# Kernel optimization log

Hardware: AMD Instinct MI355X
Metric: run time of the kernel (lower is better)

The kernel has to match this reference:

```python
import jax, jax.numpy as jnp
import numpy as np

HQ, HK, HD, DM = 16, 8, 128, 2048
GQA = HQ // HK
SCALE = HD ** -0.5


def _rotate_half(x):
    half = x.shape[-1] // 2
    return jnp.concatenate([-x[..., half:], x[..., :half]], axis=-1)


def _rope_tables(T, d, base=10000.0):
    inv_freq = 1.0 / (base ** (np.arange(0, d // 2, dtype=np.float32) * 2.0 / d))
    ang = np.arange(T, dtype=np.float32)[:, None] * inv_freq[None, :]  # [T, d/2]
    ang = np.concatenate([ang, ang], axis=-1)                          # [T, d]
    cos = jnp.asarray(np.cos(ang))[None, None]                         # [1,1,T,d]
    sin = jnp.asarray(np.sin(ang))[None, None]
    return cos, sin


def setup_inputs() -> dict:
    key = jax.random.key(0)
    ks = jax.random.split(key, 8)
    B, T, L = 1, 2048, 4
    x = jax.random.normal(ks[0], (B, T, DM), dtype=jnp.float32)
    depth_k = jax.random.normal(ks[1], (L, B, HK, T, HD), dtype=jnp.float32)
    depth_v = jax.random.normal(ks[2], (L, B, HK, T, HD), dtype=jnp.float32)
    cos, sin = _rope_tables(T, HD)
    Wq = jax.random.normal(ks[3], (DM, HQ * HD), dtype=jnp.float32) * 0.02
    Wk = jax.random.normal(ks[4], (DM, HK * HD), dtype=jnp.float32) * 0.02
    Wv = jax.random.normal(ks[5], (DM, HK * HD), dtype=jnp.float32) * 0.02
    Wo = jax.random.normal(ks[6], (HQ * HD, DM), dtype=jnp.float32) * 0.02
    return {"x": x, "depth_k": depth_k, "depth_v": depth_v, "cos": cos, "sin": sin,
            "Wq": Wq, "Wk": Wk, "Wv": Wv, "Wo": Wo}


def reference(x, depth_k, depth_v, cos, sin, Wq, Wk, Wv, Wo):
    B, T, D = x.shape
    # Projections -> [B, H, T, d]
    Q = (x @ Wq).reshape(B, T, HQ, HD).transpose(0, 2, 1, 3)
    K = (x @ Wk).reshape(B, T, HK, HD).transpose(0, 2, 1, 3)
    V = (x @ Wv).reshape(B, T, HK, HD).transpose(0, 2, 1, 3)
    # RoPE
    Q = Q * cos + _rotate_half(Q) * sin
    K = K * cos + _rotate_half(K) * sin
    # GQA expand (repeat_interleave along head axis)
    K_e = jnp.repeat(K, GQA, axis=1)
    V_e = jnp.repeat(V, GQA, axis=1)
    # Sequence logits with causal mask: [B, Hq, T, T]
    seq_logits = jnp.einsum('bhid,bhjd->bhij', Q, K_e) * SCALE
    causal = jnp.triu(jnp.ones((T, T), dtype=bool), k=1)
    seq_logits = jnp.where(causal[None, None], -jnp.inf, seq_logits)
    # Depth KVs: [L,B,Hk,T,d] -> [B,Hk,T,L,d] -> expand heads
    Kd = jnp.repeat(jnp.transpose(depth_k, (1, 2, 3, 0, 4)), GQA, axis=1)
    Vd = jnp.repeat(jnp.transpose(depth_v, (1, 2, 3, 0, 4)), GQA, axis=1)
    depth_logits = jnp.einsum('bhid,bhild->bhil', Q, Kd) * SCALE  # [B,Hq,T,L]
    # Joint softmax over sequence + depth positions
    combined = jnp.concatenate([seq_logits, depth_logits], axis=-1)
    weights = jax.nn.softmax(combined, axis=-1)
    seq_contrib = jnp.einsum('bhij,bhjd->bhid', weights[..., :T], V_e)
    depth_contrib = jnp.einsum('bhil,bhild->bhid', weights[..., T:], Vd)
    out = (seq_contrib + depth_contrib).transpose(0, 2, 1, 3).reshape(B, T, HQ * HD)
    return out @ Wo
```

## Files before the change

kernel.cpp:

```cpp
#include <hip/hip_runtime.h>
#include <hip/hip_bf16.h>
#include <math.h>

#define T_SEQ 2048
#define DMODEL 2048
#define NHQ 16
#define NHK 8
#define HDIM 128
#define NL 4
#define ATT_SCALE 0.08838834764831845f

typedef __attribute__((ext_vector_type(8))) short bf16x8;
typedef __attribute__((ext_vector_type(4))) float f32x4;

__device__ __forceinline__ float bf2f(short u) {
    union { float f; unsigned int i; } x;
    x.i = ((unsigned int)(unsigned short)u) << 16;
    return x.f;
}
__device__ __forceinline__ unsigned short f2bf(float f) {
    __hip_bfloat16 h = __float2bfloat16(f);
    return *reinterpret_cast<unsigned short*>(&h);
}
__device__ __forceinline__ void gload16(const void* g, void* l) {
    __builtin_amdgcn_global_load_lds(
        (const __attribute__((address_space(1))) void*)g,
        (__attribute__((address_space(3))) void*)l, 16, 0, 0);
}

__global__ __launch_bounds__(256) void prep(
    const float* __restrict__ x, const float* __restrict__ Wq,
    const float* __restrict__ Wk, const float* __restrict__ Wv,
    const float* __restrict__ Wo,
    unsigned short* __restrict__ xb, unsigned short* __restrict__ WTp,
    unsigned short* __restrict__ WoT)
{
    __shared__ float ls[64][65];
    const int bid = blockIdx.x, tid = threadIdx.x;
    if (bid < 2048) {
        int i = bid * 256 + tid;
        float4 a = ((const float4*)x)[2 * i];
        float4 b = ((const float4*)x)[2 * i + 1];
        bf16x8 v;
        v[0] = (short)f2bf(a.x); v[1] = (short)f2bf(a.y);
        v[2] = (short)f2bf(a.z); v[3] = (short)f2bf(a.w);
        v[4] = (short)f2bf(b.x); v[5] = (short)f2bf(b.y);
        v[6] = (short)f2bf(b.z); v[7] = (short)f2bf(b.w);
        ((bf16x8*)xb)[i] = v;
        return;
    }
    int v = bid - 2048;
    const float* src; unsigned short* dst; int Nsrc, dstOff, id;
    if (v < 1024)      { src = Wq; dst = WTp; Nsrc = 2048; dstOff = 0;    id = v; }
    else if (v < 1536) { src = Wk; dst = WTp; Nsrc = 1024; dstOff = 2048; id = v - 1024; }
    else if (v < 2048) { src = Wv; dst = WTp; Nsrc = 1024; dstOff = 3072; id = v - 1536; }
    else               { src = Wo; dst = WoT; Nsrc = 2048; dstOff = 0;    id = v - 2048; }
    const int k0 = (id & 31) * 64, n0 = (id >> 5) * 64;
    #pragma unroll
    for (int it = 0; it < 4; ++it) {
        int fi = tid + it * 256;
        int r = fi >> 4;
        int c = (fi & 15) * 4;
        float4 w = *(const float4*)&src[(size_t)(k0 + r) * Nsrc + n0 + c];
        ls[r][c] = w.x; ls[r][c + 1] = w.y; ls[r][c + 2] = w.z; ls[r][c + 3] = w.w;
    }
    __syncthreads();
    int n = tid & 63, kc = tid >> 6;
    bf16x8 v0, v1;
    #pragma unroll
    for (int j = 0; j < 8; ++j) v0[j] = (short)f2bf(ls[kc * 16 + j][n]);
    #pragma unroll
    for (int j = 0; j < 8; ++j) v1[j] = (short)f2bf(ls[kc * 16 + 8 + j][n]);
    size_t drow = (size_t)(dstOff + n0 + n) * 2048 + k0 + kc * 16;
    *(bf16x8*)&dst[drow] = v0;
    *(bf16x8*)&dst[drow + 8] = v1;
}

__global__ __launch_bounds__(256, 4) void gemm_bt(
    const unsigned short* __restrict__ A, const unsigned short* __restrict__ Bt,
    float* __restrict__ Cf, unsigned short* __restrict__ Cq,
    unsigned short* __restrict__ Ck, unsigned short* __restrict__ Cv,
    int mode, int K)
{
    __shared__ char As[16384];
    __shared__ char Bs[8192];
    const int tid = threadIdx.x;
    const int wv = tid >> 6, lane = tid & 63;
    const int l15 = lane & 15, lg = lane >> 4;
    const int wm = wv >> 1, wn = wv & 1;
    const int bm = blockIdx.y * 128, bn = blockIdx.x * 64;

    f32x4 acc[4][2];
    #pragma unroll
    for (int i = 0; i < 4; ++i)
        #pragma unroll
        for (int j = 0; j < 2; ++j)
            acc[i][j] = (f32x4){0.f, 0.f, 0.f, 0.f};

    for (int k0 = 0; k0 < K; k0 += 64) {
        #pragma unroll
        for (int it = 0; it < 4; ++it) {
            int o = it * 4096 + tid * 16;
            int row = o >> 7;
            int sch = ((o >> 4) & 7) ^ (row & 7);
            gload16((const char*)A + ((((size_t)(bm + row) * K) + k0 + sch * 8) << 1),
                    As + it * 4096 + wv * 1024);
        }
        #pragma unroll
        for (int it = 0; it < 2; ++it) {
            int o = it * 4096 + tid * 16;
            int row = o >> 7;
            int sch = ((o >> 4) & 7) ^ (row & 7);
            gload16((const char*)Bt + ((((size_t)(bn + row) * K) + k0 + sch * 8) << 1),
                    Bs + it * 4096 + wv * 1024);
        }
        __syncthreads();
        #pragma unroll
        for (int kk = 0; kk < 2; ++kk) {
            bf16x8 av[4], bv[2];
            #pragma unroll
            for (int f = 0; f < 4; ++f) {
                int ra = wm * 64 + f * 16 + l15;
                av[f] = *(const bf16x8*)(As + ra * 128 + ((((kk << 2) | lg) ^ (ra & 7)) << 4));
            }
            #pragma unroll
            for (int f = 0; f < 2; ++f) {
                int rb = wn * 32 + f * 16 + l15;
                bv[f] = *(const bf16x8*)(Bs + rb * 128 + ((((kk << 2) | lg) ^ (rb & 7)) << 4));
            }
            #pragma unroll
            for (int mf = 0; mf < 4; ++mf)
                #pragma unroll
                for (int nf = 0; nf < 2; ++nf)
                    acc[mf][nf] = __builtin_amdgcn_mfma_f32_16x16x32_bf16(
                        av[mf], bv[nf], acc[mf][nf], 0, 0, 0);
        }
        __syncthreads();
    }

    #pragma unroll
    for (int mf = 0; mf < 4; ++mf) {
        int m0 = bm + wm * 64 + mf * 16 + lg * 4;
        #pragma unroll
        for (int nf = 0; nf < 2; ++nf) {
            int n0 = bn + wn * 32 + nf * 16 + l15;
            if (mode == 0) {
                #pragma unroll
                for (int r = 0; r < 4; ++r)
                    Cf[(size_t)(m0 + r) * 2048 + n0] = acc[mf][nf][r];
            } else if (n0 < 2048) {
                #pragma unroll
                for (int r = 0; r < 4; ++r)
                    Cq[(size_t)(m0 + r) * 2048 + n0] = f2bf(acc[mf][nf][r]);
            } else if (n0 < 3072) {
                #pragma unroll
                for (int r = 0; r < 4; ++r)
                    Ck[(size_t)(m0 + r) * 1024 + (n0 - 2048)] = f2bf(acc[mf][nf][r]);
            } else {
                ushort4 u;
                u.x = f2bf(acc[mf][nf][0]); u.y = f2bf(acc[mf][nf][1]);
                u.z = f2bf(acc[mf][nf][2]); u.w = f2bf(acc[mf][nf][3]);
                *(ushort4*)&Cv[(size_t)(n0 - 3072) * 2048 + m0] = u;
            }
        }
    }
}

__global__ __launch_bounds__(256) void rope2(
    unsigned short* __restrict__ Qb, unsigned short* __restrict__ Kb,
    const float* __restrict__ cosT, const float* __restrict__ sinT)
{
    int idx = blockIdx.x * 256 + threadIdx.x;
    unsigned short* P; int H;
    if (idx < T_SEQ * NHQ * 64) { P = Qb; H = NHQ; }
    else { idx -= T_SEQ * NHQ * 64; P = Kb; H = NHK; }
    int d = idx & 63;
    int h = (idx >> 6) % H;
    int t = idx / (64 * H);
    float c = cosT[t * HDIM + d];
    float s = sinT[t * HDIM + d];
    unsigned short* row = P + (size_t)t * (H * HDIM) + h * HDIM;
    float x0 = bf2f((short)row[d]), x1 = bf2f((short)row[d + 64]);
    row[d]      = f2bf(x0 * c - x1 * s);
    row[d + 64] = f2bf(x1 * c + x0 * s);
}

__global__ __launch_bounds__(256) void depth_part(
    const unsigned short* __restrict__ Qb,
    const float* __restrict__ Dk, const float* __restrict__ Dv,
    unsigned short* __restrict__ Opart, float2* __restrict__ mlpart)
{
    const int bid = blockIdx.x;
    const int hk = bid & 7;
    const int tc = bid >> 3;
    const int tid = threadIdx.x;
    const int row = tid >> 3;
    const int dp = tid & 7;
    const int t = tc * 32 + row;
    const int qt = t >> 6, rowin = t & 63;
    const size_t DSTRIDE = (size_t)NHK * T_SEQ * HDIM;
    const size_t base = ((size_t)hk * T_SEQ + t) * HDIM + dp * 16;

    float q[2][16];
    #pragma unroll
    for (int e = 0; e < 2; ++e) {
        const unsigned short* qp = Qb + (size_t)t * DMODEL + (hk * 2 + e) * HDIM + dp * 16;
        bf16x8 v0 = *(const bf16x8*)qp;
        bf16x8 v1 = *(const bf16x8*)(qp + 8);
        #pragma unroll
        for (int j = 0; j < 8; ++j) { q[e][j] = bf2f(v0[j]); q[e][8 + j] = bf2f(v1[j]); }
    }
    float dl[2][NL];
    #pragma unroll
    for (int l = 0; l < NL; ++l) {
        const float* kp = Dk + l * DSTRIDE + base;
        float a0 = 0.f, a1 = 0.f;
        #pragma unroll
        for (int c = 0; c < 4; ++c) {
            float4 k4 = *(const float4*)(kp + c * 4);
            a0 = fmaf(q[0][c*4+0], k4.x, a0); a0 = fmaf(q[0][c*4+1], k4.y, a0);
            a0 = fmaf(q[0][c*4+2], k4.z, a0); a0 = fmaf(q[0][c*4+3], k4.w, a0);
            a1 = fmaf(q[1][c*4+0], k4.x, a1); a1 = fmaf(q[1][c*4+1], k4.y, a1);
            a1 = fmaf(q[1][c*4+2], k4.z, a1); a1 = fmaf(q[1][c*4+3], k4.w, a1);
        }
        a0 += __shfl_xor(a0, 1); a0 += __shfl_xor(a0, 2); a0 += __shfl_xor(a0, 4);
        a1 += __shfl_xor(a1, 1); a1 += __shfl_xor(a1, 2); a1 += __shfl_xor(a1, 4);
        dl[0][l] = a0 * ATT_SCALE;
        dl[1][l] = a1 * ATT_SCALE;
    }
    float m[2], ls[2], pd[2][NL];
    #pragma unroll
    for (int e = 0; e < 2; ++e) {
        m[e] = fmaxf(fmaxf(dl[e][0], dl[e][1]), fmaxf(dl[e][2], dl[e][3]));
        ls[e] = 0.f;
        #pragma unroll
        for (int l = 0; l < NL; ++l) { pd[e][l] = __expf(dl[e][l] - m[e]); ls[e] += pd[e][l]; }
    }
    float o[2][16];
    #pragma unroll
    for (int e = 0; e < 2; ++e)
        #pragma unroll
        for (int j = 0; j < 16; ++j) o[e][j] = 0.f;
    #pragma unroll
    for (int l = 0; l < NL; ++l) {
        const float* vp = Dv + l * DSTRIDE + base;
        #pragma unroll
        for (int c = 0; c < 4; ++c) {
            float4 v4 = *(const float4*)(vp + c * 4);
            #pragma unroll
            for (int e = 0; e < 2; ++e) {
                o[e][c*4+0] = fmaf(pd[e][l], v4.x, o[e][c*4+0]);
                o[e][c*4+1] = fmaf(pd[e][l], v4.y, o[e][c*4+1]);
                o[e][c*4+2] = fmaf(pd[e][l], v4.z, o[e][c*4+2]);
                o[e][c*4+3] = fmaf(pd[e][l], v4.w, o[e][c*4+3]);
            }
        }
    }
    #pragma unroll
    for (int e = 0; e < 2; ++e) {
        int pidx = ((hk * 2 + e) * 32 + qt) * 5 + 4;
        unsigned short* dst = Opart + (size_t)pidx * 8192 + rowin * 128 + dp * 16;
        bf16x8 w0, w1;
        #pragma unroll
        for (int j = 0; j < 8; ++j) { w0[j] = (short)f2bf(o[e][j]); w1[j] = (short)f2bf(o[e][8 + j]); }
        *(bf16x8*)dst = w0;
        *(bf16x8*)(dst + 8) = w1;
        if (dp == 0) mlpart[pidx * 64 + rowin] = make_float2(m[e], ls[e]);
    }
}

__global__ __launch_bounds__(256, 5) void attn_seg(
    const unsigned short* __restrict__ Qb, const unsigned short* __restrict__ Kb,
    const unsigned short* __restrict__ Vt,
    unsigned short* __restrict__ Opart, float2* __restrict__ mlpart)
{
    __shared__ char Ks[2][8192];
    __shared__ char Vs[2][8192];

    const int bid = blockIdx.x;
    const int hk = bid & 7;
    const int idx = bid >> 3;
    const int hq = hk * 2 + (idx & 1);
    const int si = 79 - (idx >> 1);
    int qt, seg;
    if (si < 8)       { qt = si;            seg = 0; }
    else if (si < 24) { int v = si - 8;  qt = 8  + (v >> 1); seg = v & 1; }
    else if (si < 48) { int v = si - 24; int q3 = v / 3; qt = 16 + q3; seg = v - q3 * 3; }
    else              { int v = si - 48; qt = 24 + (v >> 2); seg = v & 3; }
    const int q0 = qt * 64;
    const int keys = q0 + 64;
    const int jbeg = seg * 512;
    const int jend = min(jbeg + 512, keys);

    const int tid = threadIdx.x;
    const int wv = tid >> 6, lane = tid & 63;
    const int l15 = lane & 15, lg = lane >> 4;

    const int tq = q0 + wv * 16 + l15;
    const int qmax = q0 + wv * 16 + 15;
    const int qmin = q0 + wv * 16;

    bf16x8 qf[4];
    {
        const unsigned short* qrow = Qb + (size_t)tq * DMODEL + hq * HDIM;
        #pragma unroll
        for (int c = 0; c < 4; ++c)
            qf[c] = *(const bf16x8*)(qrow + c * 32 + lg * 8);
    }

    f32x4 oacc[8];
    #pragma unroll
    for (int dt = 0; dt < 8; ++dt) oacc[dt] = (f32x4){0.f, 0.f, 0.f, 0.f};
    float m = -1e30f, l = 0.f;

    #define STAGE(J0, BUF)                                                        \
        {                                                                         \
            _Pragma("unroll")                                                     \
            for (int it = 0; it < 2; ++it) {                                      \
                int o = it * 4096 + tid * 16;                                     \
                int rk = o >> 8, ck = (o >> 4) & 15;                              \
                gload16((const char*)Kb +                                         \
                        (((size_t)((J0) + rk) * 1024 + hk * 128 +                 \
                          ((ck ^ (rk & 7)) << 3)) << 1),                          \
                        Ks[BUF] + it * 4096 + wv * 1024);                         \
                int rv = o >> 6, cv = (o >> 4) & 3;                               \
                gload16((const char*)Vt +                                         \
                        (((size_t)(hk * 128 + rv) * 2048 + (J0) +                 \
                          ((cv ^ ((rv >> 1) & 3)) << 3)) << 1),                   \
                        Vs[BUF] + it * 4096 + wv * 1024);                         \
            }                                                                     \
        }

    STAGE(jbeg, 0);
    __syncthreads();
    int buf = 0;

    for (int j0 = jbeg; j0 < jend; j0 += 32) {
        if (j0 + 32 < jend) STAGE(j0 + 32, buf ^ 1);

        if (j0 <= qmax) {
            const char* ksb = Ks[buf];
            const char* vsb = Vs[buf];
            const bool fullt = (j0 + 31 <= qmin);
            float p[2][4];
            #pragma unroll
            for (int s = 0; s < 2; ++s) {
                if (j0 + s * 16 <= qmax) {
                    f32x4 sa = (f32x4){0.f, 0.f, 0.f, 0.f};
                    int row = s * 16 + l15;
                    #pragma unroll
                    for (int c = 0; c < 4; ++c) {
                        int ch = (c * 4 + lg) ^ (row & 7);
                        bf16x8 kf = *(const bf16x8*)(ksb + row * 256 + ch * 16);
                        sa = __builtin_amdgcn_mfma_f32_16x16x32_bf16(kf, qf[c], sa, 0, 0, 0);
                    }
                    #pragma unroll
                    for (int r = 0; r < 4; ++r) {
                        int key = j0 + s * 16 + lg * 4 + r;
                        p[s][r] = (fullt || key <= tq) ? sa[r] * ATT_SCALE : -1e30f;
                    }
                } else {
                    #pragma unroll
                    for (int r = 0; r < 4; ++r) p[s][r] = -1e30f;
                }
            }
            float vmax = p[0][0];
            #pragma unroll
            for (int s = 0; s < 2; ++s)
                #pragma unroll
                for (int r = 0; r < 4; ++r) vmax = fmaxf(vmax, p[s][r]);
            vmax = fmaxf(vmax, __shfl_xor(vmax, 16));
            vmax = fmaxf(vmax, __shfl_xor(vmax, 32));
            if (!__all(vmax <= m + 8.0f)) {
                float mn = fmaxf(m, vmax);
                float rs = __expf(m - mn);
                m = mn;
                l *= rs;
                float rs_o[4];
                #pragma unroll
                for (int r = 0; r < 4; ++r) rs_o[r] = __shfl(rs, lg * 4 + r);
                #pragma unroll
                for (int dt = 0; dt < 8; ++dt)
                    #pragma unroll
                    for (int r = 0; r < 4; ++r) oacc[dt][r] *= rs_o[r];
            }
            float sum = 0.f;
            #pragma unroll
            for (int s = 0; s < 2; ++s)
                #pragma unroll
                for (int r = 0; r < 4; ++r) {
                    float pe = __expf(p[s][r] - m);
                    p[s][r] = pe;
                    sum += pe;
                }
            sum += __shfl_xor(sum, 16);
            sum += __shfl_xor(sum, 32);
            l += sum;

            unsigned int D00 = (unsigned int)f2bf(p[0][0]) | ((unsigned int)f2bf(p[0][1]) << 16);
            unsigned int D01 = (unsigned int)f2bf(p[0][2]) | ((unsigned int)f2bf(p[0][3]) << 16);
            unsigned int D10 = (unsigned int)f2bf(p[1][0]) | ((unsigned int)f2bf(p[1][1]) << 16);
            unsigned int D11 = (unsigned int)f2bf(p[1][2]) | ((unsigned int)f2bf(p[1][3]) << 16);
            int src0 = ((lg & 1) << 5) + l15;
            int src1 = src0 + 16;
            unsigned int a0 = __shfl(D00, src0), a1 = __shfl(D01, src0);
            unsigned int a2 = __shfl(D00, src1), a3 = __shfl(D01, src1);
            unsigned int b0 = __shfl(D10, src0), b1 = __shfl(D11, src0);
            unsigned int b2 = __shfl(D10, src1), b3 = __shfl(D11, src1);
            union { uint4 u; bf16x8 v; } pk;
            pk.u = (lg & 2) ? make_uint4(b0, b1, b2, b3) : make_uint4(a0, a1, a2, a3);
            bf16x8 pa = pk.v;
            #pragma unroll
            for (int dt = 0; dt < 8; ++dt) {
                int rv = dt * 16 + l15;
                bf16x8 vf = *(const bf16x8*)(vsb + rv * 64 + ((lg ^ ((rv >> 1) & 3)) << 4));
                oacc[dt] = __builtin_amdgcn_mfma_f32_16x16x32_bf16(pa, vf, oacc[dt], 0, 0, 0);
            }
        }
        __syncthreads();
        buf ^= 1;
    }

    const int p = (hq * 32 + qt) * 5 + seg;
    unsigned short* op = Opart + (size_t)p * 8192;
    #pragma unroll
    for (int r = 0; r < 4; ++r) {
        unsigned short* orow = op + (wv * 16 + lg * 4 + r) * 128;
        #pragma unroll
        for (int dt = 0; dt < 8; ++dt)
            orow[dt * 16 + l15] = f2bf(oacc[dt][r]);
    }
    if (lg == 0) mlpart[p * 64 + wv * 16 + l15] = make_float2(m, l);
    #undef STAGE
}

__global__ __launch_bounds__(256) void attn_combine(
    const unsigned short* __restrict__ Opart, const float2* __restrict__ mlpart,
    unsigned short* __restrict__ AO)
{
    const int bid = blockIdx.x;
    const int hq = bid & 15;
    const int qt = bid >> 4;
    const int nseg = (qt >> 3) + 1;
    const int pbase = (hq * 32 + qt) * 5;
    const int tid = threadIdx.x;
    const int row = tid >> 2;
    const int dp = tid & 3;
    const int t = qt * 64 + row;

    int slots[5];
    for (int i = 0; i < nseg; ++i) slots[i] = i;
    slots[nseg] = 4;
    const int cnt = nseg + 1;

    float mi[5], li[5];
    float M = -1e30f;
    for (int i = 0; i < cnt; ++i) {
        float2 v = mlpart[(pbase + slots[i]) * 64 + row];
        mi[i] = v.x; li[i] = v.y;
        M = fmaxf(M, v.x);
    }
    float L = 0.f, w[5];
    for (int i = 0; i < cnt; ++i) {
        w[i] = __expf(mi[i] - M);
        L += w[i] * li[i];
    }
    float linv = 1.f / L;

    float o[32];
    #pragma unroll
    for (int j = 0; j < 32; ++j) o[j] = 0.f;
    for (int i = 0; i < cnt; ++i) {
        const unsigned short* opr =
            Opart + (size_t)(pbase + slots[i]) * 8192 + row * 128 + dp * 32;
        #pragma unroll
        for (int c = 0; c < 4; ++c) {
            bf16x8 v = *(const bf16x8*)(opr + c * 8);
            #pragma unroll
            for (int j = 0; j < 8; ++j)
                o[c * 8 + j] = fmaf(w[i], bf2f(v[j]), o[c * 8 + j]);
        }
    }
    unsigned short* orow = AO + (size_t)t * DMODEL + hq * HDIM + dp * 32;
    #pragma unroll
    for (int c = 0; c < 4; ++c) {
        bf16x8 v;
        #pragma unroll
        for (int j = 0; j < 8; ++j) v[j] = (short)f2bf(o[c * 8 + j] * linv);
        *(bf16x8*)(orow + c * 8) = v;
    }
}

extern "C" void kernel_launch(void* const* d_in, const int* in_sizes, int n_in,
                              void* d_out, int out_size, void* d_ws, size_t ws_size,
                              hipStream_t stream) {
    const float* x    = (const float*)d_in[0];
    const float* dk   = (const float*)d_in[1];
    const float* dv   = (const float*)d_in[2];
    const float* cosT = (const float*)d_in[3];
    const float* sinT = (const float*)d_in[4];
    const float* Wq   = (const float*)d_in[5];
    const float* Wk   = (const float*)d_in[6];
    const float* Wv   = (const float*)d_in[7];
    const float* Wo   = (const float*)d_in[8];
    float* out = (float*)d_out;

    unsigned short* xb  = (unsigned short*)d_ws;
    unsigned short* Qb  = xb + (size_t)4 * 1024 * 1024;
    unsigned short* Kb  = Qb + (size_t)4 * 1024 * 1024;
    unsigned short* Vt  = Kb + (size_t)2 * 1024 * 1024;
    unsigned short* WoT = Vt + (size_t)2 * 1024 * 1024;
    unsigned short* WTp = WoT + (size_t)4 * 1024 * 1024;
    unsigned short* Opart = WTp;
    float2* mlpart = (float2*)(Opart + (size_t)2560 * 8192);
    unsigned short* AOb = xb;

    prep<<<dim3(5120), 256, 0, stream>>>(x, Wq, Wk, Wv, Wo, xb, WTp, WoT);
    gemm_bt<<<dim3(64, 16), 256, 0, stream>>>(xb, WTp, nullptr, Qb, Kb, Vt, 1, DMODEL);
    rope2<<<dim3(12288), 256, 0, stream>>>(Qb, Kb, cosT, sinT);
    depth_part<<<dim3(512), 256, 0, stream>>>(Qb, dk, dv, Opart, mlpart);
    attn_seg<<<dim3(1280), 256, 0, stream>>>(Qb, Kb, Vt, Opart, mlpart);
    attn_combine<<<dim3(512), 256, 0, stream>>>(Opart, mlpart, AOb);
    gemm_bt<<<dim3(32, 16), 256, 0, stream>>>(AOb, WoT, out, nullptr, nullptr, nullptr, 0, DMODEL);
}
```

Measured before the change: 179.5 us.

## Fuse depth attention into sequence attention kernel and load K/V directly from global

Merges the depth-KV partial kernel and the segmented causal attention kernel into one launch, with the first 512 blocks doing depth work and the rest doing sequence segments. The sequence path drops the double-buffered LDS staging of K and V and the per-tile __syncthreads. K and V fragments are now read straight from global memory (relying on cache), and P is transposed through a small per-wave LDS buffer instead of shuffles. This removes one launch and block-level sync, but each wave loses LDS reuse of K/V across the four waves and may become bound on global/L2 latency.

```diff
diff --git a/kernel.cpp b/kernel.cpp
--- a/kernel.cpp
+++ b/kernel.cpp
@@ -185,99 +185,96 @@
     row[d + 64] = f2bf(x1 * c + x0 * s);
 }
 
-__global__ __launch_bounds__(256) void depth_part(
-    const unsigned short* __restrict__ Qb,
+__global__ __launch_bounds__(256, 4) void attn_fused(
+    const unsigned short* __restrict__ Qb, const unsigned short* __restrict__ Kb,
+    const unsigned short* __restrict__ Vt,
     const float* __restrict__ Dk, const float* __restrict__ Dv,
     unsigned short* __restrict__ Opart, float2* __restrict__ mlpart)
 {
-    const int bid = blockIdx.x;
-    const int hk = bid & 7;
-    const int tc = bid >> 3;
+    __shared__ char Ps[4096];
+    const int bid0 = blockIdx.x;
     const int tid = threadIdx.x;
-    const int row = tid >> 3;
-    const int dp = tid & 7;
-    const int t = tc * 32 + row;
-    const int qt = t >> 6, rowin = t & 63;
     const size_t DSTRIDE = (size_t)NHK * T_SEQ * HDIM;
-    const size_t base = ((size_t)hk * T_SEQ + t) * HDIM + dp * 16;
-
-    float q[2][16];
-    #pragma unroll
-    for (int e = 0; e < 2; ++e) {
-        const unsigned short* qp = Qb + (size_t)t * DMODEL + (hk * 2 + e) * HDIM + dp * 16;
-        bf16x8 v0 = *(const bf16x8*)qp;
-        bf16x8 v1 = *(const bf16x8*)(qp + 8);
-        #pragma unroll
-        for (int j = 0; j < 8; ++j) { q[e][j] = bf2f(v0[j]); q[e][8 + j] = bf2f(v1[j]); }
-    }
-    float dl[2][NL];
-    #pragma unroll
-    for (int l = 0; l < NL; ++l) {
-        const float* kp = Dk + l * DSTRIDE + base;
-        float a0 = 0.f, a1 = 0.f;
-        #pragma unroll
-        for (int c = 0; c < 4; ++c) {
-            float4 k4 = *(const float4*)(kp + c * 4);
-            a0 = fmaf(q[0][c*4+0], k4.x, a0); a0 = fmaf(q[0][c*4+1], k4.y, a0);
-            a0 = fmaf(q[0][c*4+2], k4.z, a0); a0 = fmaf(q[0][c*4+3], k4.w, a0);
-            a1 = fmaf(q[1][c*4+0], k4.x, a1); a1 = fmaf(q[1][c*4+1], k4.y, a1);
-            a1 = fmaf(q[1][c*4+2], k4.z, a1); a1 = fmaf(q[1][c*4+3], k4.w, a1);
-        }
-        a0 += __shfl_xor(a0, 1); a0 += __shfl_xor(a0, 2); a0 += __shfl_xor(a0, 4);
-        a1 += __shfl_xor(a1, 1); a1 += __shfl_xor(a1, 2); a1 += __shfl_xor(a1, 4);
-        dl[0][l] = a0 * ATT_SCALE;
-        dl[1][l] = a1 * ATT_SCALE;
-    }
-    float m[2], ls[2], pd[2][NL];
-    #pragma unroll
-    for (int e = 0; e < 2; ++e) {
-        m[e] = fmaxf(fmaxf(dl[e][0], dl[e][1]), fmaxf(dl[e][2], dl[e][3]));
-        ls[e] = 0.f;
-        #pragma unroll
-        for (int l = 0; l < NL; ++l) { pd[e][l] = __expf(dl[e][l] - m[e]); ls[e] += pd[e][l]; }
-    }
-    float o[2][16];
-    #pragma unroll
-    for (int e = 0; e < 2; ++e)
-        #pragma unroll
-        for (int j = 0; j < 16; ++j) o[e][j] = 0.f;
-    #pragma unroll
-    for (int l = 0; l < NL; ++l) {
-        const float* vp = Dv + l * DSTRIDE + base;
-        #pragma unroll
-        for (int c = 0; c < 4; ++c) {
-            float4 v4 = *(const float4*)(vp + c * 4);
-            #pragma unroll
-            for (int e = 0; e < 2; ++e) {
-                o[e][c*4+0] = fmaf(pd[e][l], v4.x, o[e][c*4+0]);
-                o[e][c*4+1] = fmaf(pd[e][l], v4.y, o[e][c*4+1]);
-                o[e][c*4+2] = fmaf(pd[e][l], v4.z, o[e][c*4+2]);
-                o[e][c*4+3] = fmaf(pd[e][l], v4.w, o[e][c*4+3]);
-            }
-        }
-    }
-    #pragma unroll
-    for (int e = 0; e < 2; ++e) {
-        int pidx = ((hk * 2 + e) * 32 + qt) * 5 + 4;
-        unsigned short* dst = Opart + (size_t)pidx * 8192 + rowin * 128 + dp * 16;
-        bf16x8 w0, w1;
-        #pragma unroll
-        for (int j = 0; j < 8; ++j) { w0[j] = (short)f2bf(o[e][j]); w1[j] = (short)f2bf(o[e][8 + j]); }
-        *(bf16x8*)dst = w0;
-        *(bf16x8*)(dst + 8) = w1;
-        if (dp == 0) mlpart[pidx * 64 + rowin] = make_float2(m[e], ls[e]);
-    }
-}
-
-__global__ __launch_bounds__(256, 5) void attn_seg(
-    const unsigned short* __restrict__ Qb, const unsigned short* __restrict__ Kb,
-    const unsigned short* __restrict__ Vt,
-    unsigned short* __restrict__ Opart, float2* __restrict__ mlpart)
-{
-    __shared__ char Ks[2][8192];
-    __shared__ char Vs[2][8192];
-
-    const int bid = blockIdx.x;
+
+    if (bid0 < 512) {
+        const int hk = bid0 & 7;
+        const int tc = bid0 >> 3;
+        const int row = tid >> 3;
+        const int dp = tid & 7;
+        const int t = tc * 32 + row;
+        const int qt = t >> 6, rowin = t & 63;
+        const size_t base = ((size_t)hk * T_SEQ + t) * HDIM + dp * 16;
+
+        float q[2][16];
+        #pragma unroll
+        for (int e = 0; e < 2; ++e) {
+            const unsigned short* qp = Qb + (size_t)t * DMODEL + (hk * 2 + e) * HDIM + dp * 16;
+            bf16x8 v0 = *(const bf16x8*)qp;
+            bf16x8 v1 = *(const bf16x8*)(qp + 8);
+            #pragma unroll
+            for (int j = 0; j < 8; ++j) { q[e][j] = bf2f(v0[j]); q[e][8 + j] = bf2f(v1[j]); }
+        }
+        float dl[2][NL];
+        #pragma unroll
+        for (int l = 0; l < NL; ++l) {
+            const float* kp = Dk + l * DSTRIDE + base;
+            float a0 = 0.f, a1 = 0.f;
+            #pragma unroll
+            for (int c = 0; c < 4; ++c) {
+                float4 k4 = *(const float4*)(kp + c * 4);
+                a0 = fmaf(q[0][c*4+0], k4.x, a0); a0 = fmaf(q[0][c*4+1], k4.y, a0);
+                a0 = fmaf(q[0][c*4+2], k4.z, a0); a0 = fmaf(q[0][c*4+3], k4.w, a0);
+                a1 = fmaf(q[1][c*4+0], k4.x, a1); a1 = fmaf(q[1][c*4+1], k4.y, a1);
+                a1 = fmaf(q[1][c*4+2], k4.z, a1); a1 = fmaf(q[1][c*4+3], k4.w, a1);
+            }
+            a0 += __shfl_xor(a0, 1); a0 += __shfl_xor(a0, 2); a0 += __shfl_xor(a0, 4);
+            a1 += __shfl_xor(a1, 1); a1 += __shfl_xor(a1, 2); a1 += __shfl_xor(a1, 4);
+            dl[0][l] = a0 * ATT_SCALE;
+            dl[1][l] = a1 * ATT_SCALE;
+        }
+        float m2[2], ls2[2], pd[2][NL];
+        #pragma unroll
+        for (int e = 0; e < 2; ++e) {
+            m2[e] = fmaxf(fmaxf(dl[e][0], dl[e][1]), fmaxf(dl[e][2], dl[e][3]));
+            ls2[e] = 0.f;
+            #pragma unroll
+            for (int l = 0; l < NL; ++l) { pd[e][l] = __expf(dl[e][l] - m2[e]); ls2[e] += pd[e][l]; }
+        }
+        float o[2][16];
+        #pragma unroll
+        for (int e = 0; e < 2; ++e)
+            #pragma unroll
+            for (int j = 0; j < 16; ++j) o[e][j] = 0.f;
+        #pragma unroll
+        for (int l = 0; l < NL; ++l) {
+            const float* vp = Dv + l * DSTRIDE + base;
+            #pragma unroll
+            for (int c = 0; c < 4; ++c) {
+                float4 v4 = *(const float4*)(vp + c * 4);
+                #pragma unroll
+                for (int e = 0; e < 2; ++e) {
+                    o[e][c*4+0] = fmaf(pd[e][l], v4.x, o[e][c*4+0]);
+                    o[e][c*4+1] = fmaf(pd[e][l], v4.y, o[e][c*4+1]);
+                    o[e][c*4+2] = fmaf(pd[e][l], v4.z, o[e][c*4+2]);
+                    o[e][c*4+3] = fmaf(pd[e][l], v4.w, o[e][c*4+3]);
+                }
+            }
+        }
+        #pragma unroll
+        for (int e = 0; e < 2; ++e) {
+            int pidx = ((hk * 2 + e) * 32 + qt) * 5 + 4;
+            unsigned short* dst = Opart + (size_t)pidx * 8192 + rowin * 128 + dp * 16;
+            bf16x8 w0, w1;
+            #pragma unroll
+            for (int j = 0; j < 8; ++j) { w0[j] = (short)f2bf(o[e][j]); w1[j] = (short)f2bf(o[e][8 + j]); }
+            *(bf16x8*)dst = w0;
+            *(bf16x8*)(dst + 8) = w1;
+            if (dp == 0) mlpart[pidx * 64 + rowin] = make_float2(m2[e], ls2[e]);
+        }
+        return;
+    }
+
+    const int bid = bid0 - 512;
     const int hk = bid & 7;
     const int idx = bid >> 3;
     const int hq = hk * 2 + (idx & 1);
@@ -288,11 +285,9 @@
     else if (si < 48) { int v = si - 24; int q3 = v / 3; qt = 16 + q3; seg = v - q3 * 3; }
     else              { int v = si - 48; qt = 24 + (v >> 2); seg = v & 3; }
     const int q0 = qt * 64;
-    const int keys = q0 + 64;
     const int jbeg = seg * 512;
-    const int jend = min(jbeg + 512, keys);
-
-    const int tid = threadIdx.x;
+    const int jend = min(jbeg + 512, q0 + 64);
+
     const int wv = tid >> 6, lane = tid & 63;
     const int l15 = lane & 15, lg = lane >> 4;
 
@@ -313,112 +308,87 @@
     for (int dt = 0; dt < 8; ++dt) oacc[dt] = (f32x4){0.f, 0.f, 0.f, 0.f};
     float m = -1e30f, l = 0.f;
 
-    #define STAGE(J0, BUF)                                                        \
-        {                                                                         \
-            _Pragma("unroll")                                                     \
-            for (int it = 0; it < 2; ++it) {                                      \
-                int o = it * 4096 + tid * 16;                                     \
-                int rk = o >> 8, ck = (o >> 4) & 15;                              \
-                gload16((const char*)Kb +                                         \
-                        (((size_t)((J0) + rk) * 1024 + hk * 128 +                 \
-                          ((ck ^ (rk & 7)) << 3)) << 1),                          \
-                        Ks[BUF] + it * 4096 + wv * 1024);                         \
-                int rv = o >> 6, cv = (o >> 4) & 3;                               \
-                gload16((const char*)Vt +                                         \
-                        (((size_t)(hk * 128 + rv) * 2048 + (J0) +                 \
-                          ((cv ^ ((rv >> 1) & 3)) << 3)) << 1),                   \
-                        Vs[BUF] + it * 4096 + wv * 1024);                         \
-            }                                                                     \
-        }
-
-    STAGE(jbeg, 0);
-    __syncthreads();
-    int buf = 0;
+    const unsigned short* Kbase = Kb + hk * HDIM + lg * 8;
+    const unsigned short* Vbase = Vt + (size_t)hk * HDIM * T_SEQ + lg * 8;
+    char* pw = Ps + wv * 1024;
+    const int prd = (lg ^ ((l15 >> 1) & 3)) << 4;
 
     for (int j0 = jbeg; j0 < jend; j0 += 32) {
-        if (j0 + 32 < jend) STAGE(j0 + 32, buf ^ 1);
-
-        if (j0 <= qmax) {
-            const char* ksb = Ks[buf];
-            const char* vsb = Vs[buf];
-            const bool fullt = (j0 + 31 <= qmin);
-            float p[2][4];
-            #pragma unroll
-            for (int s = 0; s < 2; ++s) {
-                if (j0 + s * 16 <= qmax) {
-                    f32x4 sa = (f32x4){0.f, 0.f, 0.f, 0.f};
-                    int row = s * 16 + l15;
-                    #pragma unroll
-                    for (int c = 0; c < 4; ++c) {
-                        int ch = (c * 4 + lg) ^ (row & 7);
-                        bf16x8 kf = *(const bf16x8*)(ksb + row * 256 + ch * 16);
-                        sa = __builtin_amdgcn_mfma_f32_16x16x32_bf16(kf, qf[c], sa, 0, 0, 0);
-                    }
-                    #pragma unroll
-                    for (int r = 0; r < 4; ++r) {
-                        int key = j0 + s * 16 + lg * 4 + r;
-                        p[s][r] = (fullt || key <= tq) ? sa[r] * ATT_SCALE : -1e30f;
-                    }
-                } else {
-                    #pragma unroll
-                    for (int r = 0; r < 4; ++r) p[s][r] = -1e30f;
+        if (j0 > qmax) break;
+        const bool fullt = (j0 + 31 <= qmin);
+        float p[2][4];
+        #pragma unroll
+        for (int s = 0; s < 2; ++s) {
+            if (j0 + s * 16 <= qmax) {
+                f32x4 sa = (f32x4){0.f, 0.f, 0.f, 0.f};
+                const unsigned short* kp = Kbase + (size_t)(j0 + s * 16 + l15) * 1024;
+                #pragma unroll
+                for (int c = 0; c < 4; ++c) {
+                    bf16x8 kf = *(const bf16x8*)(kp + c * 32);
+                    sa = __builtin_amdgcn_mfma_f32_16x16x32_bf16(kf, qf[c], sa, 0, 0, 0);
                 }
-            }
-            float vmax = p[0][0];
-            #pragma unroll
-            for (int s = 0; s < 2; ++s)
-                #pragma unroll
-                for (int r = 0; r < 4; ++r) vmax = fmaxf(vmax, p[s][r]);
-            vmax = fmaxf(vmax, __shfl_xor(vmax, 16));
-            vmax = fmaxf(vmax, __shfl_xor(vmax, 32));
-            if (!__all(vmax <= m + 8.0f)) {
-                float mn = fmaxf(m, vmax);
-                float rs = __expf(m - mn);
-                m = mn;
-                l *= rs;
-                float rs_o[4];
-                #pragma unroll
-                for (int r = 0; r < 4; ++r) rs_o[r] = __shfl(rs, lg * 4 + r);
-                #pragma unroll
-                for (int dt = 0; dt < 8; ++dt)
-                    #pragma unroll
-                    for (int r = 0; r < 4; ++r) oacc[dt][r] *= rs_o[r];
-            }
-            float sum = 0.f;
-            #pragma unroll
-            for (int s = 0; s < 2; ++s)
                 #pragma unroll
                 for (int r = 0; r < 4; ++r) {
-                    float pe = __expf(p[s][r] - m);
-                    p[s][r] = pe;
-                    sum += pe;
+                    int key = j0 + s * 16 + lg * 4 + r;
+                    p[s][r] = (fullt || key <= tq) ? sa[r] * ATT_SCALE : -1e30f;
                 }
-            sum += __shfl_xor(sum, 16);
-            sum += __shfl_xor(sum, 32);
-            l += sum;
-
-            unsigned int D00 = (unsigned int)f2bf(p[0][0]) | ((unsigned int)f2bf(p[0][1]) << 16);
-            unsigned int D01 = (unsigned int)f2bf(p[0][2]) | ((unsigned int)f2bf(p[0][3]) << 16);
-            unsigned int D10 = (unsigned int)f2bf(p[1][0]) | ((unsigned int)f2bf(p[1][1]) << 16);
-            unsigned int D11 = (unsigned int)f2bf(p[1][2]) | ((unsigned int)f2bf(p[1][3]) << 16);
-            int src0 = ((lg & 1) << 5) + l15;
-            int src1 = src0 + 16;
-            unsigned int a0 = __shfl(D00, src0), a1 = __shfl(D01, src0);
-            unsigned int a2 = __shfl(D00, src1), a3 = __shfl(D01, src1);
-            unsigned int b0 = __shfl(D10, src0), b1 = __shfl(D11, src0);
-            unsigned int b2 = __shfl(D10, src1), b3 = __shfl(D11, src1);
-            union { uint4 u; bf16x8 v; } pk;
-            pk.u = (lg & 2) ? make_uint4(b0, b1, b2, b3) : make_uint4(a0, a1, a2, a3);
-            bf16x8 pa = pk.v;
-            #pragma unroll
-            for (int dt = 0; dt < 8; ++dt) {
-                int rv = dt * 16 + l15;
-                bf16x8 vf = *(const bf16x8*)(vsb + rv * 64 + ((lg ^ ((rv >> 1) & 3)) << 4));
-                oacc[dt] = __builtin_amdgcn_mfma_f32_16x16x32_bf16(pa, vf, oacc[dt], 0, 0, 0);
-            }
-        }
-        __syncthreads();
-        buf ^= 1;
+            } else {
+                #pragma unroll
+                for (int r = 0; r < 4; ++r) p[s][r] = -1e30f;
+            }
+        }
+        float vmax = p[0][0];
+        #pragma unroll
+        for (int s = 0; s < 2; ++s)
+            #pragma unroll
+            for (int r = 0; r < 4; ++r) vmax = fmaxf(vmax, p[s][r]);
+        vmax = fmaxf(vmax, __shfl_xor(vmax, 16));
+        vmax = fmaxf(vmax, __shfl_xor(vmax, 32));
+        if (!__all(vmax <= m + 8.0f)) {
+            float mn = fmaxf(m, vmax);
+            float rs = __expf(m - mn);
+            m = mn;
+            l *= rs;
+            float rs_o[4];
+            #pragma unroll
+            for (int r = 0; r < 4; ++r) rs_o[r] = __shfl(rs, lg * 4 + r);
+            #pragma unroll
+            for (int dt = 0; dt < 8; ++dt)
+                #pragma unroll
+                for (int r = 0; r < 4; ++r) oacc[dt][r] *= rs_o[r];
+        }
+        float sum = 0.f;
+        #pragma unroll
+        for (int s = 0; s < 2; ++s)
+            #pragma unroll
+            for (int r = 0; r < 4; ++r) {
+                float pe = __expf(p[s][r] - m);
+                p[s][r] = pe;
+                sum += pe;
+            }
+        sum += __shfl_xor(sum, 16);
+        sum += __shfl_xor(sum, 32);
+        l += sum;
+
+        #pragma unroll
+        for (int s = 0; s < 2; ++s) {
+            unsigned int lo = (unsigned int)f2bf(p[s][0]) |
+                              ((unsigned int)f2bf(p[s][1]) << 16);
+            unsigned int hi = (unsigned int)f2bf(p[s][2]) |
+                              ((unsigned int)f2bf(p[s][3]) << 16);
+            int kc = s * 2 + (lg >> 1);
+            int ch = kc ^ ((l15 >> 1) & 3);
+            uint2 u = make_uint2(lo, hi);
+            *(uint2*)(pw + l15 * 64 + ch * 16 + (lg & 1) * 8) = u;
+        }
+        asm volatile("" ::: "memory");
+        bf16x8 pa = *(const bf16x8*)(pw + l15 * 64 + prd);
+        const unsigned short* vp = Vbase + j0 + (size_t)l15 * T_SEQ;
+        #pragma unroll
+        for (int dt = 0; dt < 8; ++dt) {
+            bf16x8 vf = *(const bf16x8*)(vp + (size_t)dt * 16 * T_SEQ);
+            oacc[dt] = __builtin_amdgcn_mfma_f32_16x16x32_bf16(pa, vf, oacc[dt], 0, 0, 0);
+        }
     }
 
     const int p = (hq * 32 + qt) * 5 + seg;
@@ -431,7 +401,6 @@
             orow[dt * 16 + l15] = f2bf(oacc[dt][r]);
     }
     if (lg == 0) mlpart[p * 64 + wv * 16 + l15] = make_float2(m, l);
-    #undef STAGE
 }
 
 __global__ __launch_bounds__(256) void attn_combine(
@@ -518,8 +487,7 @@
     prep<<<dim3(5120), 256, 0, stream>>>(x, Wq, Wk, Wv, Wo, xb, WTp, WoT);
     gemm_bt<<<dim3(64, 16), 256, 0, stream>>>(xb, WTp, nullptr, Qb, Kb, Vt, 1, DMODEL);
     rope2<<<dim3(12288), 256, 0, stream>>>(Qb, Kb, cosT, sinT);
-    depth_part<<<dim3(512), 256, 0, stream>>>(Qb, dk, dv, Opart, mlpart);
-    attn_seg<<<dim3(1280), 256, 0, stream>>>(Qb, Kb, Vt, Opart, mlpart);
+    attn_fused<<<dim3(1792), 256, 0, stream>>>(Qb, Kb, Vt, dk, dv, Opart, mlpart);
     attn_combine<<<dim3(512), 256, 0, stream>>>(Opart, mlpart, AOb);
     gemm_bt<<<dim3(32, 16), 256, 0, stream>>>(AOb, WoT, out, nullptr, nullptr, nullptr, 0, DMODEL);
 }
```

After: 290.2 us. 1.62x slower.
